# Performance work log

Hardware: AMD Instinct MI355X
Metric: run time of the kernel (lower is better)

Reference implementation:

```python
import jax, jax.numpy as jnp
import numpy as np

T, L, D, P, H = 1024, 32, 512, 512, 2048
EPS = 1e-5  # torch LayerNorm default eps


def _layer_norm(x, g, b):
    m = x.mean(axis=-1, keepdims=True)
    v = ((x - m) ** 2).mean(axis=-1, keepdims=True)
    return (x - m) * jax.lax.rsqrt(v + EPS) * g + b


def setup_inputs() -> dict:
    key = jax.random.key(0)
    ks = jax.random.split(key, 16)
    s = 0.02
    inp = {
        "base_prompts": jax.random.normal(ks[0], (T, L, D), jnp.float32),
        "new_prompt": jax.random.normal(ks[1], (L, D), jnp.float32),
        "task_embedding": jax.random.normal(ks[2], (D,), jnp.float32),
        # linear weights stored (in, out) so forward is x @ W + b
        "Wt": jax.random.normal(ks[3], (D, P), jnp.float32) * s,
        "bt": jnp.zeros((P,), jnp.float32),
        "Wq": jax.random.normal(ks[4], (D, P), jnp.float32) * s,
        "bq": jnp.zeros((P,), jnp.float32),
        "Wk": jax.random.normal(ks[5], (D, P), jnp.float32) * s,
        "bk": jnp.zeros((P,), jnp.float32),
        "Wv": jax.random.normal(ks[6], (D, P), jnp.float32) * s,
        "bv": jnp.zeros((P,), jnp.float32),
        "Wo": jax.random.normal(ks[7], (P, D), jnp.float32) * s,
        "bo": jnp.zeros((D,), jnp.float32),
        "Wa1": jax.random.normal(ks[8], (D, H), jnp.float32) * s,
        "ba1": jnp.zeros((H,), jnp.float32),
        "Wa2": jax.random.normal(ks[9], (H, D), jnp.float32) * s,
        "ba2": jnp.zeros((D,), jnp.float32),
        "g_in": jnp.ones((D,), jnp.float32),
        "b_in": jnp.zeros((D,), jnp.float32),
        "g_out": jnp.ones((D,), jnp.float32),
        "b_out": jnp.zeros((D,), jnp.float32),
    }
    return inp


def reference(base_prompts, new_prompt, task_embedding,
              Wt, bt, Wq, bq, Wk, bk, Wv, bv, Wo, bo,
              Wa1, ba1, Wa2, ba2, g_in, b_in, g_out, b_out):
    scale = 1.0 / np.sqrt(P).astype(np.float32)

    # --- task conditioning ---
    task_vec = jnp.tanh(task_embedding @ Wt + bt)                 # [P]
    key_repr = (base_prompts @ Wk + bk).mean(axis=1)              # [T,P]
    scores = (key_repr @ task_vec) * scale                        # [T]
    task_weights = jax.nn.softmax(scores)
    conditioned = base_prompts * (1.0 + task_weights[:, None, None])  # [T,L,D]

    query = new_prompt @ Wq + bq                                  # [L,P]
    keys = conditioned @ Wk + bk                                  # [T,L,P]
    values = conditioned @ Wv + bv                                # [T,L,P]

    # --- task-level attention ---
    pooled_q = query.mean(axis=0)                                 # [P]
    pooled_k = keys.mean(axis=1)                                  # [T,P]
    task_attn = jax.nn.softmax((pooled_k @ pooled_q) * scale)     # [T]
    task_weights = 0.5 * task_weights + 0.5 * task_attn
    task_weights = task_weights / jnp.maximum(task_weights.sum(), 1e-6)

    # --- enhanced mode: weighted pooling over tasks ---
    weighted_values = jnp.einsum('t,tlp->lp', task_weights, values)       # [L,P]
    weighted_keys = jnp.einsum('t,tlp->lp', task_weights, keys)           # [L,P]
    weighted_prompts = jnp.einsum('t,tld->ld', task_weights, conditioned) # [L,D]

    # --- feature-level attention ---
    feature_logits = (query @ weighted_keys.T) * scale            # [L,L]
    feature_attn = jax.nn.softmax(feature_logits, axis=-1)
    evolved_proj = feature_attn @ weighted_values                 # [L,P]

    evolved = evolved_proj @ Wo + bo                              # [L,D]
    evolved = _layer_norm(weighted_prompts + evolved, g_in, b_in)
    mlp = jax.nn.relu(evolved @ Wa1 + ba1) @ Wa2 + ba2
    aligned = _layer_norm(evolved + mlp, g_out, b_out)            # [L,D]

    aligned_prompts = jnp.broadcast_to(aligned, (T, L, D))        # stack of identical aligned prompts
    return aligned, aligned_prompts, task_weights, feature_attn
```

## Files before the change

kernel.cpp:

```cpp
#include <hip/hip_runtime.h>


static constexpr int T_ = 1024, L_ = 32, D_ = 512, P_ = 512, H_ = 2048;
static constexpr float SCALE = 0.04419417382415922f;
static constexpr float EPS_ = 1e-5f;

static constexpr int OFFO_AL = 0;
static constexpr int OFFO_AP = 16384;
static constexpr int OFFO_TW = 16384 + 16777216;
static constexpr int OFFO_FA = OFFO_TW + 1024;

static constexpr int OFF_AQP     = 0;
static constexpr int OFF_QUERY   = 67584;
static constexpr int OFF_WKTV    = 83968;
static constexpr int OFF_WKPQ    = 84480;
static constexpr int OFF_SC      = 84992;
static constexpr int OFF_U       = 85056;
static constexpr int OFF_V       = 86080;
static constexpr int OFF_PART    = 87104;
static constexpr int OFF_WB      = 611392;
static constexpr int OFF_AKVP    = 627776;
static constexpr int OFF_LG      = 758848;
static constexpr int OFF_AEVOP   = 759872;
static constexpr int OFF_EVOLVED = 890944;
static constexpr int OFF_AH1P    = 907328;
static constexpr int OFF_AOUTP   = 1169472;
static constexpr int OFF_DUMMY   = 1431616;

__device__ __forceinline__ float wred64(float v) {
    #pragma unroll
    for (int off = 32; off > 0; off >>= 1) v += __shfl_down(v, off, 64);
    return v;
}
__device__ __forceinline__ float wmax64(float v) {
    #pragma unroll
    for (int off = 32; off > 0; off >>= 1) v = fmaxf(v, __shfl_down(v, off, 64));
    return v;
}
__device__ __forceinline__ float bsum512(float v, float* buf, int tid) {
    v = wred64(v);
    __syncthreads();
    if ((tid & 63) == 0) buf[tid >> 6] = v;
    __syncthreads();
    float s = 0.f;
    #pragma unroll
    for (int i = 0; i < 8; ++i) s += buf[i];
    return s;
}
__device__ __forceinline__ float bsum128(float v, float* buf, int tid) {
    v = wred64(v);
    __syncthreads();
    if ((tid & 63) == 0) buf[tid >> 6] = v;
    __syncthreads();
    return buf[0] + buf[1];
}
__device__ __forceinline__ float bmax128(float v, float* buf, int tid) {
    v = wmax64(v);
    __syncthreads();
    if ((tid & 63) == 0) buf[tid >> 6] = v;
    __syncthreads();
    return fmaxf(buf[0], buf[1]);
}

__global__ __launch_bounds__(512) void k_aq(
    const float* __restrict__ np_, const float* __restrict__ te,
    const float* __restrict__ Wq, const float* __restrict__ Wt,
    const float* __restrict__ Wv, const float* __restrict__ Wo,
    const float* __restrict__ Wa1, const float* __restrict__ Wa2,
    float* __restrict__ ws)
{
    __shared__ float sx[128];
    int blk = blockIdx.x, tid = threadIdx.x;
    if (blk < 132) {
        int b = blk % 33, kc = blk / 33;
        const float* x = (b < 32) ? (np_ + b * D_) : te;
        const float* W = (b < 32) ? Wq : Wt;
        if (tid < 128) sx[tid] = x[kc * 128 + tid];
        __syncthreads();
        float acc = 0.f;
        #pragma unroll 8
        for (int j = 0; j < 128; ++j) acc = fmaf(sx[j], W[(kc * 128 + j) * P_ + tid], acc);
        ws[OFF_AQP + (kc * 33 + b) * P_ + tid] = acc;
    } else {
        int pw = blk - 132;
        const float* src;
        if (pw < 16)       src = Wo  + pw * 16384;
        else if (pw < 80)  src = Wa1 + (pw - 16) * 16384;
        else if (pw < 144) src = Wa2 + (pw - 80) * 16384;
        else               src = Wv  + (pw - 144) * 16384;
        const float4* s4 = (const float4*)src;
        float4 acc = make_float4(0.f, 0.f, 0.f, 0.f);
        #pragma unroll
        for (int i = 0; i < 8; ++i) {
            float4 v = s4[i * 512 + tid];
            acc.x += v.x; acc.y += v.y; acc.z += v.z; acc.w += v.w;
        }
        ws[OFF_DUMMY + pw * 512 + tid] = acc.x + acc.y + acc.z + acc.w;
    }
}

__global__ __launch_bounds__(512) void k_prep(
    const float* __restrict__ Wk, const float* __restrict__ bk,
    const float* __restrict__ bq, const float* __restrict__ bt,
    float* __restrict__ ws)
{
    __shared__ __align__(16) float stv[512];
    __shared__ __align__(16) float spq[512];
    __shared__ float buf[8];
    int blk = blockIdx.x, tid = threadIdx.x;

    float a = 0.f;
    #pragma unroll
    for (int kc = 0; kc < 4; ++kc) a += ws[OFF_AQP + (kc * 33 + 32) * P_ + tid];
    stv[tid] = tanhf(a + bt[tid]);

    float b = 0.f;
    #pragma unroll 4
    for (int kc = 0; kc < 4; ++kc)
        for (int l = 0; l < 32; ++l) b += ws[OFF_AQP + (kc * 33 + l) * P_ + tid];
    spq[tid] = b * (1.f / 32.f) + bq[tid];

    if (blk < 32) {
        float q = bq[tid];
        #pragma unroll
        for (int kc = 0; kc < 4; ++kc) q += ws[OFF_AQP + (kc * 33 + blk) * P_ + tid];
        ws[OFF_QUERY + blk * P_ + tid] = q;
    }
    __syncthreads();

    int wv = tid >> 6, lane = tid & 63;
    int d = blk * 8 + wv;
    const float4* row = (const float4*)(Wk + d * P_);
    const float4* tv4 = (const float4*)stv;
    const float4* pq4 = (const float4*)spq;
    float4 r0 = row[lane * 2], r1 = row[lane * 2 + 1];
    float4 t0 = tv4[lane * 2], t1 = tv4[lane * 2 + 1];
    float4 q0 = pq4[lane * 2], q1 = pq4[lane * 2 + 1];
    float pa = r0.x * t0.x + r0.y * t0.y + r0.z * t0.z + r0.w * t0.w
             + r1.x * t1.x + r1.y * t1.y + r1.z * t1.z + r1.w * t1.w;
    float pb = r0.x * q0.x + r0.y * q0.y + r0.z * q0.z + r0.w * q0.w
             + r1.x * q1.x + r1.y * q1.y + r1.z * q1.z + r1.w * q1.w;
    pa = wred64(pa); pb = wred64(pb);
    if (lane == 0) { ws[OFF_WKTV + d] = pa; ws[OFF_WKPQ + d] = pb; }

    if (blk == 63) {
        float bkf = bk[tid];
        float s1 = bsum512(bkf * stv[tid], buf, tid);
        float s2 = bsum512(bkf * spq[tid], buf, tid);
        if (tid == 0) { ws[OFF_SC] = s1; ws[OFF_SC + 1] = s2; }
    }
}

__global__ __launch_bounds__(512) void k_scanuv(
    const float* __restrict__ base, float* __restrict__ ws)
{
    __shared__ __align__(16) float4 smem4[512];
    __shared__ __align__(16) float sfin[512];
    __shared__ float buf[8];
    int t = blockIdx.x, tid = threadIdx.x;
    const float4* bp = (const float4*)(base + (size_t)t * (L_ * D_));
    int d4 = tid & 127, lq = tid >> 7;
    float4 acc = make_float4(0.f, 0.f, 0.f, 0.f);
    #pragma unroll
    for (int i = 0; i < 8; ++i) {
        float4 v = bp[(i * 4 + lq) * 128 + d4];
        acc.x += v.x; acc.y += v.y; acc.z += v.z; acc.w += v.w;
    }
    smem4[tid] = acc;
    __syncthreads();
    if (tid < 128) {
        float4 a = smem4[tid], b2 = smem4[tid + 128];
        float4 c = smem4[tid + 256], d2 = smem4[tid + 384];
        float4 r;
        r.x = a.x + b2.x + c.x + d2.x;
        r.y = a.y + b2.y + c.y + d2.y;
        r.z = a.z + b2.z + c.z + d2.z;
        r.w = a.w + b2.w + c.w + d2.w;
        ((float4*)sfin)[tid] = r;
    }
    __syncthreads();
    float s = sfin[tid];
    float u = bsum512(s * ws[OFF_WKTV + tid], buf, tid);
    float v = bsum512(s * ws[OFF_WKPQ + tid], buf, tid);
    if (tid == 0) {
        ws[OFF_U + t] = u * (1.f / L_);
        ws[OFF_V + t] = v * (1.f / L_);
    }
}

__global__ __launch_bounds__(128) void k_part(
    const float* __restrict__ base, float* __restrict__ out_tw,
    float* __restrict__ ws)
{
    __shared__ float sC[1024];
    __shared__ float rbuf[2];
    int l = blockIdx.x, ch = blockIdx.y, tid = threadIdx.x;
    float bkt = ws[OFF_SC], bkq = ws[OFF_SC + 1];

    float u[8], v[8], s1[8], tw1[8], tw[8];
    #pragma unroll
    for (int i = 0; i < 8; ++i) {
        int t = i * 128 + tid;
        u[i] = ws[OFF_U + t];
        v[i] = ws[OFF_V + t];
    }
    float lmax = -1e30f;
    #pragma unroll
    for (int i = 0; i < 8; ++i) { s1[i] = (u[i] + bkt) * SCALE; lmax = fmaxf(lmax, s1[i]); }
    float gmax = bmax128(lmax, rbuf, tid);
    float ls = 0.f;
    #pragma unroll
    for (int i = 0; i < 8; ++i) { s1[i] = expf(s1[i] - gmax); ls += s1[i]; }
    float gs = bsum128(ls, rbuf, tid);
    #pragma unroll
    for (int i = 0; i < 8; ++i) tw1[i] = s1[i] / gs;
    lmax = -1e30f;
    #pragma unroll
    for (int i = 0; i < 8; ++i) {
        s1[i] = ((1.f + tw1[i]) * v[i] + bkq) * SCALE;
        lmax = fmaxf(lmax, s1[i]);
    }
    gmax = bmax128(lmax, rbuf, tid);
    ls = 0.f;
    #pragma unroll
    for (int i = 0; i < 8; ++i) { s1[i] = expf(s1[i] - gmax); ls += s1[i]; }
    gs = bsum128(ls, rbuf, tid);
    float lsum = 0.f;
    #pragma unroll
    for (int i = 0; i < 8; ++i) {
        tw[i] = 0.5f * tw1[i] + 0.5f * (s1[i] / gs);
        lsum += tw[i];
    }
    float S = bsum128(lsum, rbuf, tid);
    S = fmaxf(S, 1e-6f);
    #pragma unroll
    for (int i = 0; i < 8; ++i) {
        int t = i * 128 + tid;
        float twn = tw[i] / S;
        sC[t] = twn * (1.f + tw1[i]);
        if (l == 0 && ch == 0) out_tw[t] = twn;
    }
    __syncthreads();

    float4 acc = make_float4(0.f, 0.f, 0.f, 0.f);
    for (int i = 0; i < 32; ++i) {
        int t = ch * 32 + i;
        float c = sC[t];
        float4 bv4 = ((const float4*)(base + ((size_t)t * L_ + l) * D_))[tid];
        acc.x = fmaf(c, bv4.x, acc.x);
        acc.y = fmaf(c, bv4.y, acc.y);
        acc.z = fmaf(c, bv4.z, acc.z);
        acc.w = fmaf(c, bv4.w, acc.w);
    }
    ((float4*)(ws + OFF_PART + (ch * 32 + l) * D_))[tid] = acc;
}

__global__ __launch_bounds__(512) void k_kv(
    const float* __restrict__ Wk, const float* __restrict__ Wv,
    float* __restrict__ ws)
{
    __shared__ float part[512];
    __shared__ float sx[128];
    int blk = blockIdx.x, tid = threadIdx.x;
    int l = blk & 31, sel = (blk >> 5) & 1, kc = blk >> 6;
    int p = tid & 127, c = tid >> 7;
    float s = 0.f;
    #pragma unroll
    for (int ch = c; ch < 32; ch += 4)
        s += ws[OFF_PART + (ch * 32 + l) * D_ + kc * 128 + p];
    part[tid] = s;
    __syncthreads();
    if (tid < 128) {
        float w = part[tid] + part[tid + 128] + part[tid + 256] + part[tid + 384];
        sx[tid] = w;
        if (sel == 0) ws[OFF_WB + l * D_ + kc * 128 + tid] = w;
    }
    __syncthreads();
    const float* W = sel ? Wv : Wk;
    float acc = 0.f;
    #pragma unroll 8
    for (int j = 0; j < 128; ++j) acc = fmaf(sx[j], W[(kc * 128 + j) * P_ + tid], acc);
    ws[OFF_AKVP + ((kc * 2 + sel) * 32 + l) * P_ + tid] = acc;
}

__global__ __launch_bounds__(512) void k_logits(
    const float* __restrict__ bk, float* __restrict__ ws)
{
    __shared__ __align__(16) float sq[512];
    int l = blockIdx.x, gc = blockIdx.y, tid = threadIdx.x;
    int wv = tid >> 6, lane = tid & 63;
    sq[tid] = ws[OFF_QUERY + l * P_ + tid];
    __syncthreads();
    const float4* sq4 = (const float4*)sq;
    const float4* bk4 = (const float4*)bk;
    float4 q0 = sq4[lane * 2], q1 = sq4[lane * 2 + 1];
    float4 A = bk4[lane * 2], B = bk4[lane * 2 + 1];
    int g = gc * 4 + wv;
    #pragma unroll
    for (int kc = 0; kc < 4; ++kc) {
        const float4* kr = (const float4*)(ws + OFF_AKVP + ((kc * 2) * 32 + g) * P_);
        float4 a = kr[lane * 2], b = kr[lane * 2 + 1];
        A.x += a.x; A.y += a.y; A.z += a.z; A.w += a.w;
        B.x += b.x; B.y += b.y; B.z += b.z; B.w += b.w;
    }
    float sdot = A.x * q0.x + A.y * q0.y + A.z * q0.z + A.w * q0.w
               + B.x * q1.x + B.y * q1.y + B.z * q1.z + B.w * q1.w;
    sdot = wred64(sdot);
    if (lane == 0) ws[OFF_LG + l * 32 + g] = sdot * SCALE;
}

__global__ __launch_bounds__(512) void k_evoEP(
    const float* __restrict__ bv, const float* __restrict__ Wo,
    float* __restrict__ out_fa, float* __restrict__ ws)
{
    __shared__ float slg[32];
    __shared__ float sfa[32];
    __shared__ float pe[8][64];
    __shared__ float sx[64];
    int l = blockIdx.x, kc = blockIdx.y, tid = threadIdx.x;
    if (tid < 32) slg[tid] = ws[OFF_LG + l * 32 + tid];
    __syncthreads();
    if (tid < 32) {
        float mx = -1e30f;
        for (int i = 0; i < 32; ++i) mx = fmaxf(mx, slg[i]);
        float S = 0.f;
        for (int i = 0; i < 32; ++i) S += expf(slg[i] - mx);
        float f = expf(slg[tid] - mx) / S;
        sfa[tid] = f;
        if (kc == 0) out_fa[l * 32 + tid] = f;
    }
    __syncthreads();

    int p = tid & 63, jg = tid >> 6;
    float bvp = bv[kc * 64 + p];
    float acc = 0.f;
    #pragma unroll
    for (int jj = 0; jj < 4; ++jj) {
        int j = jg * 4 + jj;
        float vs = ws[OFF_AKVP + (1 * 32 + j) * P_ + kc * 64 + p]
                 + ws[OFF_AKVP + (3 * 32 + j) * P_ + kc * 64 + p]
                 + ws[OFF_AKVP + (5 * 32 + j) * P_ + kc * 64 + p]
                 + ws[OFF_AKVP + (7 * 32 + j) * P_ + kc * 64 + p];
        acc = fmaf(sfa[j], vs + bvp, acc);
    }
    pe[jg][p] = acc;
    __syncthreads();
    if (tid < 64) {
        float s = 0.f;
        #pragma unroll
        for (int i = 0; i < 8; ++i) s += pe[i][tid];
        sx[tid] = s;
    }
    __syncthreads();

    float a2 = 0.f;
    #pragma unroll 8
    for (int j = 0; j < 64; ++j) a2 = fmaf(sx[j], Wo[(kc * 64 + j) * D_ + tid], a2);
    ws[OFF_AEVOP + (kc * 32 + l) * D_ + tid] = a2;
}

__global__ __launch_bounds__(512) void k_lnin(
    const float* __restrict__ bo, const float* __restrict__ g_in,
    const float* __restrict__ b_in, float* __restrict__ ws)
{
    __shared__ float buf[8];
    int l = blockIdx.x, tid = threadIdx.x;
    float x = ws[OFF_WB + l * D_ + tid] + bo[tid];
    #pragma unroll
    for (int k2 = 0; k2 < 8; ++k2) x += ws[OFF_AEVOP + (k2 * 32 + l) * D_ + tid];
    float mean = bsum512(x, buf, tid) * (1.f / D_);
    float dx = x - mean;
    float var = bsum512(dx * dx, buf, tid) * (1.f / D_);
    ws[OFF_EVOLVED + l * D_ + tid] = dx * rsqrtf(var + EPS_) * g_in[tid] + b_in[tid];
}

__global__ __launch_bounds__(512) void k_mlp1(
    const float* __restrict__ Wa1, float* __restrict__ ws)
{
    __shared__ float sevo[4][512];
    int blk = blockIdx.x, tid = threadIdx.x;
    int lg = blk & 7, hc = (blk >> 3) & 3, kc = blk >> 5;
    #pragma unroll
    for (int r = 0; r < 4; ++r)
        sevo[r][tid] = ws[OFF_EVOLVED + (lg * 4 + r) * D_ + tid];
    __syncthreads();
    int h = hc * 512 + tid;
    float a0 = 0.f, a1 = 0.f, a2 = 0.f, a3 = 0.f;
    #pragma unroll 8
    for (int j = 0; j < 128; ++j) {
        float w = Wa1[(kc * 128 + j) * H_ + h];
        a0 = fmaf(sevo[0][kc * 128 + j], w, a0);
        a1 = fmaf(sevo[1][kc * 128 + j], w, a1);
        a2 = fmaf(sevo[2][kc * 128 + j], w, a2);
        a3 = fmaf(sevo[3][kc * 128 + j], w, a3);
    }
    ws[OFF_AH1P + (kc * 32 + lg * 4 + 0) * H_ + h] = a0;
    ws[OFF_AH1P + (kc * 32 + lg * 4 + 1) * H_ + h] = a1;
    ws[OFF_AH1P + (kc * 32 + lg * 4 + 2) * H_ + h] = a2;
    ws[OFF_AH1P + (kc * 32 + lg * 4 + 3) * H_ + h] = a3;
}

__global__ __launch_bounds__(512) void k_mlp2(
    const float* __restrict__ Wa2, const float* __restrict__ ba1,
    float* __restrict__ ws)
{
    __shared__ float sh[4][128];
    int blk = blockIdx.x, tid = threadIdx.x;
    int lg = blk & 7, kc = blk >> 3;
    {
        int hh = tid & 127, r = tid >> 7;
        int h = kc * 128 + hh;
        float a = ba1[h];
        #pragma unroll
        for (int k4 = 0; k4 < 4; ++k4)
            a += ws[OFF_AH1P + (k4 * 32 + lg * 4 + r) * H_ + h];
        sh[r][hh] = fmaxf(a, 0.f);
    }
    __syncthreads();
    float a0 = 0.f, a1 = 0.f, a2 = 0.f, a3 = 0.f;
    #pragma unroll 8
    for (int j = 0; j < 128; ++j) {
        float w = Wa2[(kc * 128 + j) * D_ + tid];
        a0 = fmaf(sh[0][j], w, a0);
        a1 = fmaf(sh[1][j], w, a1);
        a2 = fmaf(sh[2][j], w, a2);
        a3 = fmaf(sh[3][j], w, a3);
    }
    ws[OFF_AOUTP + (kc * 32 + lg * 4 + 0) * D_ + tid] = a0;
    ws[OFF_AOUTP + (kc * 32 + lg * 4 + 1) * D_ + tid] = a1;
    ws[OFF_AOUTP + (kc * 32 + lg * 4 + 2) * D_ + tid] = a2;
    ws[OFF_AOUTP + (kc * 32 + lg * 4 + 3) * D_ + tid] = a3;
}

__global__ __launch_bounds__(512) void k_lnbcast(
    const float* __restrict__ ba2, const float* __restrict__ g_out,
    const float* __restrict__ b_out, float* __restrict__ out,
    float* __restrict__ ws)
{
    __shared__ float buf[8];
    __shared__ __align__(16) float sal[512];
    int l = blockIdx.x, tc = blockIdx.y, tid = threadIdx.x;
    float x2 = ws[OFF_EVOLVED + l * D_ + tid] + ba2[tid];
    #pragma unroll
    for (int kc = 0; kc < 16; ++kc) x2 += ws[OFF_AOUTP + (kc * 32 + l) * D_ + tid];
    float mean2 = bsum512(x2, buf, tid) * (1.f / D_);
    float dx2 = x2 - mean2;
    float var2 = bsum512(dx2 * dx2, buf, tid) * (1.f / D_);
    float a = dx2 * rsqrtf(var2 + EPS_) * g_out[tid] + b_out[tid];
    if (tc == 0) out[OFFO_AL + l * D_ + tid] = a;
    sal[tid] = a;
    __syncthreads();
    float4 v = ((const float4*)sal)[tid & 127];
    int row = tid >> 7;
    #pragma unroll
    for (int pass = 0; pass < 8; ++pass) {
        int t = tc * 32 + pass * 4 + row;
        ((float4*)(out + OFFO_AP + (size_t)t * (L_ * D_) + l * D_))[tid & 127] = v;
    }
}

extern "C" void kernel_launch(void* const* d_in, const int* in_sizes, int n_in,
                              void* d_out, int out_size, void* d_ws, size_t ws_size,
                              hipStream_t stream) {
    const float* base = (const float*)d_in[0];
    const float* np   = (const float*)d_in[1];
    const float* te   = (const float*)d_in[2];
    const float* Wt   = (const float*)d_in[3];
    const float* bt   = (const float*)d_in[4];
    const float* Wq   = (const float*)d_in[5];
    const float* bq   = (const float*)d_in[6];
    const float* Wk   = (const float*)d_in[7];
    const float* bk   = (const float*)d_in[8];
    const float* Wv   = (const float*)d_in[9];
    const float* bv   = (const float*)d_in[10];
    const float* Wo   = (const float*)d_in[11];
    const float* bo   = (const float*)d_in[12];
    const float* Wa1  = (const float*)d_in[13];
    const float* ba1  = (const float*)d_in[14];
    const float* Wa2  = (const float*)d_in[15];
    const float* ba2  = (const float*)d_in[16];
    const float* g_in = (const float*)d_in[17];
    const float* b_in = (const float*)d_in[18];
    const float* g_out= (const float*)d_in[19];
    const float* b_out= (const float*)d_in[20];
    float* out = (float*)d_out;
    float* ws = (float*)d_ws;

    hipLaunchKernelGGL(k_aq,      dim3(292),    dim3(512), 0, stream,
                       np, te, Wq, Wt, Wv, Wo, Wa1, Wa2, ws);
    hipLaunchKernelGGL(k_prep,    dim3(64),     dim3(512), 0, stream, Wk, bk, bq, bt, ws);
    hipLaunchKernelGGL(k_scanuv,  dim3(1024),   dim3(512), 0, stream, base, ws);
    hipLaunchKernelGGL(k_part,    dim3(32, 32), dim3(128), 0, stream, base, out + OFFO_TW, ws);
    hipLaunchKernelGGL(k_kv,      dim3(256),    dim3(512), 0, stream, Wk, Wv, ws);
    hipLaunchKernelGGL(k_logits,  dim3(32, 8),  dim3(512), 0, stream, bk, ws);
    hipLaunchKernelGGL(k_evoEP,   dim3(32, 8),  dim3(512), 0, stream, bv, Wo, out + OFFO_FA, ws);
    hipLaunchKernelGGL(k_lnin,    dim3(32),     dim3(512), 0, stream, bo, g_in, b_in, ws);
    hipLaunchKernelGGL(k_mlp1,    dim3(128),    dim3(512), 0, stream, Wa1, ws);
    hipLaunchKernelGGL(k_mlp2,    dim3(128),    dim3(512), 0, stream, Wa2, ba1, ws);
    hipLaunchKernelGGL(k_lnbcast, dim3(32, 32), dim3(512), 0, stream,
                       ba2, g_out, b_out, out, ws);
}
```

Baseline: 236.0 us.

## Fuse logits into evoEP, reduce k_part partials in-block, batch rows in k_kv

k_part now uses 512-thread blocks that cover 128 tasks each and reduce four partial sums in shared memory. That leaves 8 chunk partials instead of 32, so k_kv reads less. k_kv computes four rows per block so each weight element loaded is reused four times. The separate k_logits kernel is removed and its dot products are recomputed inside every k_evoEP block, which saves one launch and one global round trip. The cost is redundant logits work repeated across the 8 kc blocks per row.

```diff
diff --git a/kernel.cpp b/kernel.cpp
--- a/kernel.cpp
+++ b/kernel.cpp
@@ -20,7 +20,6 @@
 static constexpr int OFF_PART    = 87104;
 static constexpr int OFF_WB      = 611392;
 static constexpr int OFF_AKVP    = 627776;
-static constexpr int OFF_LG      = 758848;
 static constexpr int OFF_AEVOP   = 759872;
 static constexpr int OFF_EVOLVED = 890944;
 static constexpr int OFF_AH1P    = 907328;
@@ -47,19 +46,15 @@
     for (int i = 0; i < 8; ++i) s += buf[i];
     return s;
 }
-__device__ __forceinline__ float bsum128(float v, float* buf, int tid) {
-    v = wred64(v);
+__device__ __forceinline__ float bmax512(float v, float* buf, int tid) {
+    v = wmax64(v);
     __syncthreads();
     if ((tid & 63) == 0) buf[tid >> 6] = v;
     __syncthreads();
-    return buf[0] + buf[1];
-}
-__device__ __forceinline__ float bmax128(float v, float* buf, int tid) {
-    v = wmax64(v);
-    __syncthreads();
-    if ((tid & 63) == 0) buf[tid >> 6] = v;
-    __syncthreads();
-    return fmaxf(buf[0], buf[1]);
+    float m = buf[0];
+    #pragma unroll
+    for (int i = 1; i < 8; ++i) m = fmaxf(m, buf[i]);
+    return m;
 }
 
 __global__ __launch_bounds__(512) void k_aq(
@@ -188,138 +183,148 @@
     }
 }
 
-__global__ __launch_bounds__(128) void k_part(
+__global__ __launch_bounds__(512) void k_part(
     const float* __restrict__ base, float* __restrict__ out_tw,
     float* __restrict__ ws)
 {
     __shared__ float sC[1024];
-    __shared__ float rbuf[2];
-    int l = blockIdx.x, ch = blockIdx.y, tid = threadIdx.x;
+    __shared__ float buf[8];
+    __shared__ __align__(16) float4 s4[512];
+    int l = blockIdx.x, chg = blockIdx.y, tid = threadIdx.x;
     float bkt = ws[OFF_SC], bkq = ws[OFF_SC + 1];
 
-    float u[8], v[8], s1[8], tw1[8], tw[8];
-    #pragma unroll
-    for (int i = 0; i < 8; ++i) {
-        int t = i * 128 + tid;
+    float u[2], v[2], s1[2], tw1[2], tw[2];
+    #pragma unroll
+    for (int i = 0; i < 2; ++i) {
+        int t = i * 512 + tid;
         u[i] = ws[OFF_U + t];
         v[i] = ws[OFF_V + t];
     }
     float lmax = -1e30f;
     #pragma unroll
-    for (int i = 0; i < 8; ++i) { s1[i] = (u[i] + bkt) * SCALE; lmax = fmaxf(lmax, s1[i]); }
-    float gmax = bmax128(lmax, rbuf, tid);
+    for (int i = 0; i < 2; ++i) { s1[i] = (u[i] + bkt) * SCALE; lmax = fmaxf(lmax, s1[i]); }
+    float gmax = bmax512(lmax, buf, tid);
     float ls = 0.f;
     #pragma unroll
-    for (int i = 0; i < 8; ++i) { s1[i] = expf(s1[i] - gmax); ls += s1[i]; }
-    float gs = bsum128(ls, rbuf, tid);
-    #pragma unroll
-    for (int i = 0; i < 8; ++i) tw1[i] = s1[i] / gs;
+    for (int i = 0; i < 2; ++i) { s1[i] = expf(s1[i] - gmax); ls += s1[i]; }
+    float gs = bsum512(ls, buf, tid);
+    #pragma unroll
+    for (int i = 0; i < 2; ++i) tw1[i] = s1[i] / gs;
     lmax = -1e30f;
     #pragma unroll
-    for (int i = 0; i < 8; ++i) {
+    for (int i = 0; i < 2; ++i) {
         s1[i] = ((1.f + tw1[i]) * v[i] + bkq) * SCALE;
         lmax = fmaxf(lmax, s1[i]);
     }
-    gmax = bmax128(lmax, rbuf, tid);
+    gmax = bmax512(lmax, buf, tid);
     ls = 0.f;
     #pragma unroll
-    for (int i = 0; i < 8; ++i) { s1[i] = expf(s1[i] - gmax); ls += s1[i]; }
-    gs = bsum128(ls, rbuf, tid);
+    for (int i = 0; i < 2; ++i) { s1[i] = expf(s1[i] - gmax); ls += s1[i]; }
+    gs = bsum512(ls, buf, tid);
     float lsum = 0.f;
     #pragma unroll
-    for (int i = 0; i < 8; ++i) {
+    for (int i = 0; i < 2; ++i) {
         tw[i] = 0.5f * tw1[i] + 0.5f * (s1[i] / gs);
         lsum += tw[i];
     }
-    float S = bsum128(lsum, rbuf, tid);
+    float S = bsum512(lsum, buf, tid);
     S = fmaxf(S, 1e-6f);
     #pragma unroll
-    for (int i = 0; i < 8; ++i) {
-        int t = i * 128 + tid;
+    for (int i = 0; i < 2; ++i) {
+        int t = i * 512 + tid;
         float twn = tw[i] / S;
         sC[t] = twn * (1.f + tw1[i]);
-        if (l == 0 && ch == 0) out_tw[t] = twn;
-    }
-    __syncthreads();
-
+        if (l == 0 && chg == 0) out_tw[t] = twn;
+    }
+    __syncthreads();
+
+    int d4 = tid & 127, tq = tid >> 7;
     float4 acc = make_float4(0.f, 0.f, 0.f, 0.f);
     for (int i = 0; i < 32; ++i) {
-        int t = ch * 32 + i;
+        int t = chg * 128 + tq * 32 + i;
         float c = sC[t];
-        float4 bv4 = ((const float4*)(base + ((size_t)t * L_ + l) * D_))[tid];
+        float4 bv4 = ((const float4*)(base + ((size_t)t * L_ + l) * D_))[d4];
         acc.x = fmaf(c, bv4.x, acc.x);
         acc.y = fmaf(c, bv4.y, acc.y);
         acc.z = fmaf(c, bv4.z, acc.z);
         acc.w = fmaf(c, bv4.w, acc.w);
     }
-    ((float4*)(ws + OFF_PART + (ch * 32 + l) * D_))[tid] = acc;
+    s4[tid] = acc;
+    __syncthreads();
+    if (tid < 128) {
+        float4 a = s4[tid], b2 = s4[tid + 128], c2 = s4[tid + 256], d2 = s4[tid + 384];
+        float4 r;
+        r.x = a.x + b2.x + c2.x + d2.x;
+        r.y = a.y + b2.y + c2.y + d2.y;
+        r.z = a.z + b2.z + c2.z + d2.z;
+        r.w = a.w + b2.w + c2.w + d2.w;
+        ((float4*)(ws + OFF_PART + (chg * 32 + l) * D_))[tid] = r;
+    }
 }
 
 __global__ __launch_bounds__(512) void k_kv(
     const float* __restrict__ Wk, const float* __restrict__ Wv,
     float* __restrict__ ws)
 {
-    __shared__ float part[512];
-    __shared__ float sx[128];
-    int blk = blockIdx.x, tid = threadIdx.x;
-    int l = blk & 31, sel = (blk >> 5) & 1, kc = blk >> 6;
-    int p = tid & 127, c = tid >> 7;
+    __shared__ float sx[4][128];
+    int lg = blockIdx.x, sel = blockIdx.y, kc = blockIdx.z, tid = threadIdx.x;
+    int r = tid >> 7, p = tid & 127;
+    int l = lg * 4 + r;
     float s = 0.f;
     #pragma unroll
-    for (int ch = c; ch < 32; ch += 4)
+    for (int ch = 0; ch < 8; ++ch)
         s += ws[OFF_PART + (ch * 32 + l) * D_ + kc * 128 + p];
-    part[tid] = s;
-    __syncthreads();
-    if (tid < 128) {
-        float w = part[tid] + part[tid + 128] + part[tid + 256] + part[tid + 384];
-        sx[tid] = w;
-        if (sel == 0) ws[OFF_WB + l * D_ + kc * 128 + tid] = w;
-    }
+    sx[r][p] = s;
+    if (sel == 0) ws[OFF_WB + l * D_ + kc * 128 + p] = s;
     __syncthreads();
     const float* W = sel ? Wv : Wk;
-    float acc = 0.f;
+    float a0 = 0.f, a1 = 0.f, a2 = 0.f, a3 = 0.f;
     #pragma unroll 8
-    for (int j = 0; j < 128; ++j) acc = fmaf(sx[j], W[(kc * 128 + j) * P_ + tid], acc);
-    ws[OFF_AKVP + ((kc * 2 + sel) * 32 + l) * P_ + tid] = acc;
-}
-
-__global__ __launch_bounds__(512) void k_logits(
-    const float* __restrict__ bk, float* __restrict__ ws)
+    for (int j = 0; j < 128; ++j) {
+        float w = W[(kc * 128 + j) * P_ + tid];
+        a0 = fmaf(sx[0][j], w, a0);
+        a1 = fmaf(sx[1][j], w, a1);
+        a2 = fmaf(sx[2][j], w, a2);
+        a3 = fmaf(sx[3][j], w, a3);
+    }
+    int bi = (kc * 2 + sel) * 32 + lg * 4;
+    ws[OFF_AKVP + (bi + 0) * P_ + tid] = a0;
+    ws[OFF_AKVP + (bi + 1) * P_ + tid] = a1;
+    ws[OFF_AKVP + (bi + 2) * P_ + tid] = a2;
+    ws[OFF_AKVP + (bi + 3) * P_ + tid] = a3;
+}
+
+__global__ __launch_bounds__(512) void k_evoEP(
+    const float* __restrict__ bk, const float* __restrict__ bv,
+    const float* __restrict__ Wo, float* __restrict__ out_fa,
+    float* __restrict__ ws)
 {
     __shared__ __align__(16) float sq[512];
-    int l = blockIdx.x, gc = blockIdx.y, tid = threadIdx.x;
-    int wv = tid >> 6, lane = tid & 63;
-    sq[tid] = ws[OFF_QUERY + l * P_ + tid];
-    __syncthreads();
-    const float4* sq4 = (const float4*)sq;
-    const float4* bk4 = (const float4*)bk;
-    float4 q0 = sq4[lane * 2], q1 = sq4[lane * 2 + 1];
-    float4 A = bk4[lane * 2], B = bk4[lane * 2 + 1];
-    int g = gc * 4 + wv;
-    #pragma unroll
-    for (int kc = 0; kc < 4; ++kc) {
-        const float4* kr = (const float4*)(ws + OFF_AKVP + ((kc * 2) * 32 + g) * P_);
-        float4 a = kr[lane * 2], b = kr[lane * 2 + 1];
-        A.x += a.x; A.y += a.y; A.z += a.z; A.w += a.w;
-        B.x += b.x; B.y += b.y; B.z += b.z; B.w += b.w;
-    }
-    float sdot = A.x * q0.x + A.y * q0.y + A.z * q0.z + A.w * q0.w
-               + B.x * q1.x + B.y * q1.y + B.z * q1.z + B.w * q1.w;
-    sdot = wred64(sdot);
-    if (lane == 0) ws[OFF_LG + l * 32 + g] = sdot * SCALE;
-}
-
-__global__ __launch_bounds__(512) void k_evoEP(
-    const float* __restrict__ bv, const float* __restrict__ Wo,
-    float* __restrict__ out_fa, float* __restrict__ ws)
-{
     __shared__ float slg[32];
     __shared__ float sfa[32];
     __shared__ float pe[8][64];
     __shared__ float sx[64];
     int l = blockIdx.x, kc = blockIdx.y, tid = threadIdx.x;
-    if (tid < 32) slg[tid] = ws[OFF_LG + l * 32 + tid];
-    __syncthreads();
+    sq[tid] = ws[OFF_QUERY + l * P_ + tid];
+    __syncthreads();
+
+    int g = tid >> 4, li = tid & 15;
+    float sd = 0.f;
+    #pragma unroll 4
+    for (int e = 0; e < 32; ++e) {
+        int p = e * 16 + li;
+        float k = bk[p]
+                + ws[OFF_AKVP + (g) * P_ + p]
+                + ws[OFF_AKVP + (64 + g) * P_ + p]
+                + ws[OFF_AKVP + (128 + g) * P_ + p]
+                + ws[OFF_AKVP + (192 + g) * P_ + p];
+        sd = fmaf(k, sq[p], sd);
+    }
+    #pragma unroll
+    for (int off = 8; off > 0; off >>= 1) sd += __shfl_down(sd, off, 16);
+    if (li == 0) slg[g] = sd * SCALE;
+    __syncthreads();
+
     if (tid < 32) {
         float mx = -1e30f;
         for (int i = 0; i < 32; ++i) mx = fmaxf(mx, slg[i]);
@@ -337,10 +342,10 @@
     #pragma unroll
     for (int jj = 0; jj < 4; ++jj) {
         int j = jg * 4 + jj;
-        float vs = ws[OFF_AKVP + (1 * 32 + j) * P_ + kc * 64 + p]
-                 + ws[OFF_AKVP + (3 * 32 + j) * P_ + kc * 64 + p]
-                 + ws[OFF_AKVP + (5 * 32 + j) * P_ + kc * 64 + p]
-                 + ws[OFF_AKVP + (7 * 32 + j) * P_ + kc * 64 + p];
+        float vs = ws[OFF_AKVP + (32 + j) * P_ + kc * 64 + p]
+                 + ws[OFF_AKVP + (96 + j) * P_ + kc * 64 + p]
+                 + ws[OFF_AKVP + (160 + j) * P_ + kc * 64 + p]
+                 + ws[OFF_AKVP + (224 + j) * P_ + kc * 64 + p];
         acc = fmaf(sfa[j], vs + bvp, acc);
     }
     pe[jg][p] = acc;
@@ -486,17 +491,16 @@
     float* out = (float*)d_out;
     float* ws = (float*)d_ws;
 
-    hipLaunchKernelGGL(k_aq,      dim3(292),    dim3(512), 0, stream,
+    hipLaunchKernelGGL(k_aq,      dim3(292),      dim3(512), 0, stream,
                        np, te, Wq, Wt, Wv, Wo, Wa1, Wa2, ws);
-    hipLaunchKernelGGL(k_prep,    dim3(64),     dim3(512), 0, stream, Wk, bk, bq, bt, ws);
-    hipLaunchKernelGGL(k_scanuv,  dim3(1024),   dim3(512), 0, stream, base, ws);
-    hipLaunchKernelGGL(k_part,    dim3(32, 32), dim3(128), 0, stream, base, out + OFFO_TW, ws);
-    hipLaunchKernelGGL(k_kv,      dim3(256),    dim3(512), 0, stream, Wk, Wv, ws);
-    hipLaunchKernelGGL(k_logits,  dim3(32, 8),  dim3(512), 0, stream, bk, ws);
-    hipLaunchKernelGGL(k_evoEP,   dim3(32, 8),  dim3(512), 0, stream, bv, Wo, out + OFFO_FA, ws);
-    hipLaunchKernelGGL(k_lnin,    dim3(32),     dim3(512), 0, stream, bo, g_in, b_in, ws);
-    hipLaunchKernelGGL(k_mlp1,    dim3(128),    dim3(512), 0, stream, Wa1, ws);
-    hipLaunchKernelGGL(k_mlp2,    dim3(128),    dim3(512), 0, stream, Wa2, ba1, ws);
-    hipLaunchKernelGGL(k_lnbcast, dim3(32, 32), dim3(512), 0, stream,
+    hipLaunchKernelGGL(k_prep,    dim3(64),       dim3(512), 0, stream, Wk, bk, bq, bt, ws);
+    hipLaunchKernelGGL(k_scanuv,  dim3(1024),     dim3(512), 0, stream, base, ws);
+    hipLaunchKernelGGL(k_part,    dim3(32, 8),    dim3(512), 0, stream, base, out + OFFO_TW, ws);
+    hipLaunchKernelGGL(k_kv,      dim3(8, 2, 4),  dim3(512), 0, stream, Wk, Wv, ws);
+    hipLaunchKernelGGL(k_evoEP,   dim3(32, 8),    dim3(512), 0, stream, bk, bv, Wo, out + OFFO_FA, ws);
+    hipLaunchKernelGGL(k_lnin,    dim3(32),       dim3(512), 0, stream, bo, g_in, b_in, ws);
+    hipLaunchKernelGGL(k_mlp1,    dim3(128),      dim3(512), 0, stream, Wa1, ws);
+    hipLaunchKernelGGL(k_mlp2,    dim3(128),      dim3(512), 0, stream, Wa2, ba1, ws);
+    hipLaunchKernelGGL(k_lnbcast, dim3(32, 32),   dim3(512), 0, stream,
                        ba2, g_out, b_out, out, ws);
 }
```

After: 231.7 us. Within noise of the previous version (-1.8%).
